# Kernel optimization log

Hardware: AMD Instinct MI355X
Metric: run time of the kernel (lower is better)

The kernel has to match this reference:

```python
import jax, jax.numpy as jnp
import numpy as np
from jax import lax

EPS = 1e-5
GROUPS = 8
TDVD_RANGE = 10
SCALE = 1.0
SCALE_FACTOR = 0.5


def setup_inputs() -> dict:
    key = jax.random.key(0)
    k1, k2 = jax.random.split(key)
    x = jax.random.normal(k1, (2, 16, 64, 128, 128), dtype=jnp.float32)
    gn_weight = jnp.ones((16,), dtype=jnp.float32)
    gn_bias = jnp.zeros((16,), dtype=jnp.float32)
    threshold = jnp.ones((1,), dtype=jnp.float32)  # torch fills with 1.0
    conv_weight = jax.random.normal(k2, (16, 16, 3, 3, 3), dtype=jnp.float32) * 0.05
    return {"x": x, "gn_weight": gn_weight, "gn_bias": gn_bias,
            "threshold": threshold, "conv_weight": conv_weight}


def _group_norm(x, w, b):
    B, C, D, H, W = x.shape
    xr = x.reshape(B, GROUPS, C // GROUPS, D, H, W)
    mean = xr.mean(axis=(2, 3, 4, 5), keepdims=True)
    var = xr.var(axis=(2, 3, 4, 5), keepdims=True)
    xn = ((xr - mean) * lax.rsqrt(var + EPS)).reshape(B, C, D, H, W)
    return xn * w.reshape(1, C, 1, 1, 1) + b.reshape(1, C, 1, 1, 1)


def _tdvd_histogram(x):
    # reverseint(x * scale * scale_factor) counted into 21 bins [-10..10], as %.
    y = x * (SCALE * SCALE_FACTOR)
    v = jnp.ceil(y * (y >= 0)) + jnp.floor(y * (y <= 0))
    idx = (v + TDVD_RANGE).astype(jnp.int32)
    valid = (idx >= 0) & (idx <= 2 * TDVD_RANGE)
    hist = jnp.zeros((2 * TDVD_RANGE + 1,), jnp.float32).at[
        jnp.clip(idx, 0, 2 * TDVD_RANGE)].add(jnp.where(valid, 1.0, 0.0))
    return hist / x.size * 100.0


def _threshold_func(x, threshold):
    thr = (threshold[0] + 0.0) / SCALE  # zero_point=0, scale=1.0
    t = jnp.transpose(x, (2, 0, 1, 3, 4))  # [D,B,C,H,W]
    front, back = t[:-1], t[1:]
    d = (back - front) / thr
    d = jnp.where(jnp.abs(d) > 1.0, d, 0.0)  # Hardshrink(1.0)
    d = d * lax.stop_gradient(thr)           # .item() detaches in torch
    out = jnp.concatenate([t[:1], front + d], axis=0)
    return jnp.transpose(out, (1, 2, 0, 3, 4))


def reference(x, gn_weight, gn_bias, threshold, conv_weight):
    x = jax.nn.relu(_group_norm(x, gn_weight, gn_bias))
    hist = _tdvd_histogram(x)
    x = _threshold_func(x, threshold)
    out = lax.conv_general_dilated(
        x, conv_weight, window_strides=(1, 1, 1),
        padding=((1, 1), (1, 1), (1, 1)),
        dimension_numbers=("NCDHW", "OIDHW", "NCDHW"))
    return out, hist
```

## Files before the change

### kernel.cpp

```cpp
#include <hip/hip_runtime.h>

typedef __attribute__((ext_vector_type(8))) short short8;
typedef __attribute__((ext_vector_type(4))) float f32x4;

#define GROUP_ELEMS 2097152
#define NBLK 64

__device__ inline short f2bf(float f) {
  unsigned u = __builtin_bit_cast(unsigned, f);
  unsigned r = (u + 0x7FFFu + ((u >> 16) & 1u)) >> 16;
  return (short)r;
}

__device__ inline void gload_lds16(const void* g, void* l) {
  __builtin_amdgcn_global_load_lds(
      (const __attribute__((address_space(1))) unsigned int*)g,
      (__attribute__((address_space(3))) unsigned int*)l, 16, 0, 0);
}

__global__ __launch_bounds__(256) void k1_partials(const float* __restrict__ x,
                                                   float2* __restrict__ partials,
                                                   const float* __restrict__ wgt,
                                                   unsigned short* __restrict__ fbw2,
                                                   int* __restrict__ hist,
                                                   unsigned int* __restrict__ dummy) {
  if (blockIdx.x == 1024) {
    int t0 = threadIdx.x;
    if (t0 < 21) hist[t0] = 0;
    #pragma unroll
    for (int it = 0; it < 4; ++it) {
      int t = t0 + it * 256;
      if (t < 960) {
        int f = t >> 6, lane = t & 63;
        int kd = f / 5, c = f - kd * 5;
        int m = lane & 15, g = lane >> 4;
        int icb = (g & 1) * 8, g2 = g >> 1;
        int tap = 2 * c + g2;
        short8 v;
        #pragma unroll
        for (int j = 0; j < 8; ++j)
          v[j] = (tap <= 8) ? f2bf(wgt[m * 432 + (icb + j) * 27 + kd * 9 + tap]) : (short)0;
        *(short8*)(fbw2 + t * 8) = v;
      }
      if (t >= 960 && t < 976) dummy[t - 960] = 0;
    }
    return;
  }
  int group = blockIdx.x >> 6;
  int blk = blockIdx.x & 63;
  const float4* p = (const float4*)(x + (size_t)group * GROUP_ELEMS + (size_t)blk * 32768);
  float sum = 0.f, sq = 0.f;
  for (int i = threadIdx.x; i < 8192; i += 256) {
    float4 v = p[i];
    sum += v.x + v.y + v.z + v.w;
    sq  += v.x*v.x + v.y*v.y + v.z*v.z + v.w*v.w;
  }
  for (int off = 32; off; off >>= 1) {
    sum += __shfl_down(sum, off, 64);
    sq  += __shfl_down(sq,  off, 64);
  }
  __shared__ float2 sw[4];
  int lane = threadIdx.x & 63, wid = threadIdx.x >> 6;
  if (lane == 0) sw[wid] = make_float2(sum, sq);
  __syncthreads();
  if (threadIdx.x == 0) {
    float s = 0.f, q = 0.f;
    for (int j = 0; j < 4; ++j) { s += sw[j].x; q += sw[j].y; }
    partials[blockIdx.x] = make_float2(s, q);
  }
}

__global__ __launch_bounds__(256) void k3_norm_thresh_hist(
    const float* __restrict__ x, const float* __restrict__ gw, const float* __restrict__ gb,
    const float* __restrict__ thrp, const float2* __restrict__ partials,
    unsigned short* __restrict__ z, int* __restrict__ hist) {
  __shared__ int sh[21];
  __shared__ float4 stf[8];
  __shared__ float red[64], redq[64];
  __shared__ unsigned sd[2][256];
  int t = threadIdx.x;
  if (t < 21) sh[t] = 0;
  int b = blockIdx.x >> 9;
  if (t < 64) {
    int gloc = t >> 3, j8 = t & 7;
    const float2* pp = partials + (b * 8 + gloc) * NBLK + j8 * 8;
    float s = 0.f, q = 0.f;
    #pragma unroll
    for (int k = 0; k < 8; ++k) { float2 pv = pp[k]; s += pv.x; q += pv.y; }
    red[t] = s; redq[t] = q;
  }
  __syncthreads();
  if (t < 8) {
    float s = 0.f, q = 0.f;
    #pragma unroll
    for (int k = 0; k < 8; ++k) { s += red[t * 8 + k]; q += redq[t * 8 + k]; }
    float mean = s / (float)GROUP_ELEMS;
    float var  = q / (float)GROUP_ELEMS - mean * mean;
    float rs = rsqrtf(var + 1e-5f);
    int c0 = t * 2;
    float A0 = gw[c0] * rs,     B0 = gb[c0] - mean * A0;
    float A1 = gw[c0 + 1] * rs, B1 = gb[c0 + 1] - mean * A1;
    stf[t] = make_float4(A0, B0, A1, B1);
  }
  __syncthreads();
  int hwl = t & 31, cp = t >> 5;
  int hw0 = (blockIdx.x & 511) * 32;
  int hw = hw0 + hwl;
  float4 st = stf[cp];
  float A0 = st.x, B0 = st.y, A1 = st.z, B1 = st.w;
  float thr = thrp[0];
  int c0 = cp * 2, c1 = c0 + 1;
  const float* px0 = x + (size_t)(b * 16 + c0) * 1048576 + hw;
  const float* px1 = x + (size_t)(b * 16 + c1) * 1048576 + hw;
  unsigned* zout = (unsigned*)z;
  const unsigned zbase = (unsigned)(b * 1048576 + hw0) * 8;
  const int wi = (cp << 5) | ((hwl + 4 * cp) & 31);
  const int ri = ((t & 7) << 5) | (((t >> 3) + 4 * (t & 7)) & 31);
  int c10 = 0, c11 = 0, c12 = 0;
  float xv0 = px0[0], xv1 = px1[0];
  float xm0 = px0[16384], xm1 = px1[16384];
  float yp0 = 0.f, yp1 = 0.f;
  for (int d = 0; d < 64; ++d) {
    float n0 = 0.f, n1 = 0.f;
    if (d < 62) { n0 = px0[(d + 2) * 16384]; n1 = px1[(d + 2) * 16384]; }
    float y0 = fmaxf(fmaf(xv0, A0, B0), 0.f);
    float y1 = fmaxf(fmaf(xv1, A1, B1), 0.f);
    float v0 = ceilf(0.5f * y0);
    if (v0 == 0.f) c10++; else if (v0 == 1.f) c11++; else if (v0 == 2.f) c12++;
    else if (v0 <= 10.f) atomicAdd(&sh[(int)v0 + 10], 1);
    float v1 = ceilf(0.5f * y1);
    if (v1 == 0.f) c10++; else if (v1 == 1.f) c11++; else if (v1 == 2.f) c12++;
    else if (v1 <= 10.f) atomicAdd(&sh[(int)v1 + 10], 1);
    float z0, z1;
    if (d == 0) { z0 = y0; z1 = y1; }
    else {
      z0 = (fabsf(y0 - yp0) > thr) ? y0 : yp0;
      z1 = (fabsf(y1 - yp1) > thr) ? y1 : yp1;
    }
    unsigned u = (unsigned)(unsigned short)f2bf(z0) | ((unsigned)(unsigned short)f2bf(z1) << 16);
    sd[d & 1][wi] = u;
    __syncthreads();
    zout[zbase + d * 131072 + t] = sd[d & 1][ri];
    yp0 = y0; yp1 = y1;
    xv0 = xm0; xv1 = xm1;
    xm0 = n0; xm1 = n1;
  }
  atomicAdd(&sh[10], c10);
  atomicAdd(&sh[11], c11);
  atomicAdd(&sh[12], c12);
  __syncthreads();
  if (t < 21) atomicAdd(&hist[t], sh[t]);
}

#define DT 8
#define PLANE 5440
__global__ __launch_bounds__(512, 4) void k4_conv(const unsigned short* __restrict__ z,
                                                  const unsigned short* __restrict__ fbw2,
                                                  const char* __restrict__ dummyc,
                                                  const int* __restrict__ hist,
                                                  float* __restrict__ out) {
  __shared__ unsigned short lz[2 * PLANE];
  const int t = threadIdx.x;
  if (blockIdx.x == 0 && blockIdx.y == 0 && blockIdx.z == 0 && t < 21)
    out[33554432u + t] = (float)hist[t] * (100.0f / 33554432.0f);
  const int lane = t & 63, wid = t >> 6;
  const int b = blockIdx.z;
  const int d0 = blockIdx.y * DT;
  const int h0 = (blockIdx.x >> 2) * 8, w0 = (blockIdx.x & 3) * 32;
  const int m = lane & 15, g = lane >> 4;
  const int icb = (g & 1) * 8, g2 = g >> 1;

  short8 fb2[15];
  #pragma unroll
  for (int f = 0; f < 15; ++f)
    fb2[f] = *(const short8*)(fbw2 + (f * 64 + lane) * 8);

  int tco[5];
  #pragma unroll
  for (int c = 0; c < 5; ++c) {
    int tap = 2 * c + g2; if (tap > 8) tap = 8;
    tco[c] = ((tap / 3) * 34 + (tap % 3)) * 16;
  }

  const char* zbc = (const char*)(z + (size_t)b * 16777216);

  const int cbA = wid * 64;
  const int cbB = (wid == 0) ? 512 : (wid == 1) ? 576 : 616;
  const bool hasB = (wid < 3);
  long long hobA, hobB; bool hvA, hvB;
  {
    int gi, r, rem, s, ig, hg, wg;
    gi = cbA + lane; r = gi / 68; rem = gi - r * 68; s = rem >> 1; ig = rem & 1;
    hg = h0 - 1 + r; wg = w0 - 1 + s;
    hvA = ((unsigned)hg < 128u) && ((unsigned)wg < 128u);
    hobA = ((long long)(hg * 128 + wg) * 16 + ig * 8) * 2;
    gi = cbB + lane; r = gi / 68; rem = gi - r * 68; s = rem >> 1; ig = rem & 1;
    hg = h0 - 1 + r; wg = w0 - 1 + s;
    hvB = ((unsigned)hg < 128u) && ((unsigned)wg < 128u);
    hobB = ((long long)(hg * 128 + wg) * 16 + ig * 8) * 2;
  }

  const f32x4 fzero = {0.f, 0.f, 0.f, 0.f};
  f32x4 A0[2], A1[2], A2[2];
  #pragma unroll
  for (int q = 0; q < 2; ++q) { A0[q] = fzero; A1[q] = fzero; A2[q] = fzero; }

  {
    const int dg = d0 - 1;
    const long long dgo = (long long)dg * 524288;
    const bool pd = (unsigned)dg < 64u;
    gload_lds16((pd && hvA) ? zbc + dgo + hobA : dummyc, &lz[cbA * 8]);
    if (hasB)
      gload_lds16((pd && hvB) ? zbc + dgo + hobB : dummyc, &lz[cbB * 8]);
  }
  __syncthreads();

#define BODY(PH, AS, AM, AN, DOJ2, DOJ1, DOJ0, DOLOAD, DOSTORE)                         \
  {                                                                                     \
    const int ph_ = (PH);                                                               \
    if (DOLOAD) {                                                                       \
      const int dg = d0 + ph_;                                                          \
      const long long dgo = (long long)dg * 524288;                                     \
      const bool pd = (unsigned)dg < 64u;                                               \
      const unsigned sl = ((unsigned)(ph_ + 1) & 1u) * PLANE;                           \
      gload_lds16((pd && hvA) ? zbc + dgo + hobA : dummyc, &lz[sl + cbA * 8]);          \
      if (hasB)                                                                         \
        gload_lds16((pd && hvB) ? zbc + dgo + hobB : dummyc, &lz[sl + cbB * 8]);        \
    }                                                                                   \
    const unsigned su = ((unsigned)ph_ & 1u) * PLANE;                                   \
    __builtin_amdgcn_s_setprio(1);                                                      \
    _Pragma("unroll")                                                                   \
    for (int q = 0; q < 2; ++q) {                                                       \
      const int hl = wid, wt = q;                                                       \
      const int qb = (hl * 34 + wt * 16 + m) * 16 + icb + (int)su;                      \
      _Pragma("unroll")                                                                 \
      for (int c = 0; c < 5; ++c) {                                                     \
        short8 a = *(const short8*)(&lz[qb + tco[c]]);                                  \
        if (DOJ2) AN[q] = __builtin_amdgcn_mfma_f32_16x16x32_bf16(a, fb2[c], AN[q], 0, 0, 0);      \
        if (DOJ1) AM[q] = __builtin_amdgcn_mfma_f32_16x16x32_bf16(a, fb2[5 + c], AM[q], 0, 0, 0);  \
        if (DOJ0) AS[q] = __builtin_amdgcn_mfma_f32_16x16x32_bf16(a, fb2[10 + c], AS[q], 0, 0, 0); \
      }                                                                                 \
    }                                                                                   \
    __builtin_amdgcn_s_setprio(0);                                                      \
    if (DOSTORE) {                                                                      \
      const int dd = d0 + ph_ - 2;                                                      \
      _Pragma("unroll")                                                                 \
      for (int q = 0; q < 2; ++q) {                                                     \
        const int hl = wid, wt = q;                                                     \
        float* op = out + (((size_t)(b * 16 + m) * 64 + dd) * 128 + (h0 + hl)) * 128    \
                    + w0 + wt * 16 + g * 4;                                             \
        *(float4*)op = make_float4(AS[q][0], AS[q][1], AS[q][2], AS[q][3]);             \
        AS[q] = fzero;                                                                  \
      }                                                                                 \
    }                                                                                   \
    __syncthreads();                                                                    \
  }

  BODY(0, A1, A2, A0, 1, 0, 0, 1, 0)
  BODY(1, A2, A0, A1, 1, 1, 0, 1, 0)
  BODY(2, A0, A1, A2, 1, 1, 1, 1, 1)
  #pragma unroll 1
  for (int pp = 3; pp <= 6; pp += 3) {
    BODY(pp,     A1, A2, A0, 1, 1, 1, 1, 1)
    BODY(pp + 1, A2, A0, A1, 1, 1, 1, 1, 1)
    BODY(pp + 2, A0, A1, A2, 1, 1, 1, 1, 1)
  }
  BODY(9, A1, A2, A0, 0, 0, 1, 0, 1)
#undef BODY
}

extern "C" void kernel_launch(void* const* d_in, const int* in_sizes, int n_in,
                              void* d_out, int out_size, void* d_ws, size_t ws_size,
                              hipStream_t stream) {
  (void)in_sizes; (void)n_in; (void)out_size; (void)ws_size;
  const float* x   = (const float*)d_in[0];
  const float* gw  = (const float*)d_in[1];
  const float* gb  = (const float*)d_in[2];
  const float* thr = (const float*)d_in[3];
  const float* cw  = (const float*)d_in[4];
  float* out = (float*)d_out;

  char* ws = (char*)d_ws;
  unsigned short* z = (unsigned short*)ws;
  float2* partials  = (float2*)(ws + (size_t)67108864);
  int*    hist      = (int*)  (ws + (size_t)67108864 + 8192 + 128);
  unsigned int* dummy = (unsigned int*)(ws + (size_t)67108864 + 8448);
  unsigned short* fbw2 = (unsigned short*)(ws + (size_t)67108864 + 16384);

  k1_partials<<<1025, 256, 0, stream>>>(x, partials, cw, fbw2, hist, dummy);
  k3_norm_thresh_hist<<<1024, 256, 0, stream>>>(x, gw, gb, thr, partials, z, hist);
  k4_conv<<<dim3(64, 8, 2), 512, 0, stream>>>(z, fbw2, (const char*)dummy, hist, out);
}
```

Baseline: 122.5 us.

## Quad-buffer conv input planes and process two depth planes per barrier

Grows the LDS staging buffer from two to four depth planes and restructures the conv pipeline to load two planes and compute two planes between each block barrier. This halves the number of __syncthreads and gives more prefetch distance to hide global-to-LDS load latency. The cost is twice the LDS per block (about 43KB), which may cut the number of resident blocks below the launch_bounds target of 4.

```diff
diff --git a/kernel.cpp b/kernel.cpp
--- a/kernel.cpp
+++ b/kernel.cpp
@@ -159,7 +159,7 @@
                                                   const char* __restrict__ dummyc,
                                                   const int* __restrict__ hist,
                                                   float* __restrict__ out) {
-  __shared__ unsigned short lz[2 * PLANE];
+  __shared__ unsigned short lz[4 * PLANE];
   const int t = threadIdx.x;
   if (blockIdx.x == 0 && blockIdx.y == 0 && blockIdx.z == 0 && t < 21)
     out[33554432u + t] = (float)hist[t] * (100.0f / 33554432.0f);
@@ -205,29 +205,20 @@
   #pragma unroll
   for (int q = 0; q < 2; ++q) { A0[q] = fzero; A1[q] = fzero; A2[q] = fzero; }
 
-  {
-    const int dg = d0 - 1;
-    const long long dgo = (long long)dg * 524288;
-    const bool pd = (unsigned)dg < 64u;
-    gload_lds16((pd && hvA) ? zbc + dgo + hobA : dummyc, &lz[cbA * 8]);
-    if (hasB)
-      gload_lds16((pd && hvB) ? zbc + dgo + hobB : dummyc, &lz[cbB * 8]);
-  }
-  __syncthreads();
-
-#define BODY(PH, AS, AM, AN, DOJ2, DOJ1, DOJ0, DOLOAD, DOSTORE)                         \
+#define STAGE(P)                                                                        \
   {                                                                                     \
-    const int ph_ = (PH);                                                               \
-    if (DOLOAD) {                                                                       \
-      const int dg = d0 + ph_;                                                          \
-      const long long dgo = (long long)dg * 524288;                                     \
-      const bool pd = (unsigned)dg < 64u;                                               \
-      const unsigned sl = ((unsigned)(ph_ + 1) & 1u) * PLANE;                           \
-      gload_lds16((pd && hvA) ? zbc + dgo + hobA : dummyc, &lz[sl + cbA * 8]);          \
-      if (hasB)                                                                         \
-        gload_lds16((pd && hvB) ? zbc + dgo + hobB : dummyc, &lz[sl + cbB * 8]);        \
-    }                                                                                   \
-    const unsigned su = ((unsigned)ph_ & 1u) * PLANE;                                   \
+    const int dg = d0 - 1 + (P);                                                        \
+    const long long dgo = (long long)dg * 524288;                                       \
+    const bool pd = (unsigned)dg < 64u;                                                 \
+    const unsigned sl = ((unsigned)(P) & 3u) * PLANE;                                   \
+    gload_lds16((pd && hvA) ? zbc + dgo + hobA : dummyc, &lz[sl + cbA * 8]);            \
+    if (hasB)                                                                           \
+      gload_lds16((pd && hvB) ? zbc + dgo + hobB : dummyc, &lz[sl + cbB * 8]);          \
+  }
+
+#define PC(P, AS, AM, AN, DOJ2, DOJ1, DOJ0, DOSTORE)                                    \
+  {                                                                                     \
+    const unsigned su = ((unsigned)(P) & 3u) * PLANE;                                   \
     __builtin_amdgcn_s_setprio(1);                                                      \
     _Pragma("unroll")                                                                   \
     for (int q = 0; q < 2; ++q) {                                                       \
@@ -243,7 +234,7 @@
     }                                                                                   \
     __builtin_amdgcn_s_setprio(0);                                                      \
     if (DOSTORE) {                                                                      \
-      const int dd = d0 + ph_ - 2;                                                      \
+      const int dd = d0 + (P) - 2;                                                      \
       _Pragma("unroll")                                                                 \
       for (int q = 0; q < 2; ++q) {                                                     \
         const int hl = wid, wt = q;                                                     \
@@ -253,20 +244,30 @@
         AS[q] = fzero;                                                                  \
       }                                                                                 \
     }                                                                                   \
-    __syncthreads();                                                                    \
-  }
-
-  BODY(0, A1, A2, A0, 1, 0, 0, 1, 0)
-  BODY(1, A2, A0, A1, 1, 1, 0, 1, 0)
-  BODY(2, A0, A1, A2, 1, 1, 1, 1, 1)
-  #pragma unroll 1
-  for (int pp = 3; pp <= 6; pp += 3) {
-    BODY(pp,     A1, A2, A0, 1, 1, 1, 1, 1)
-    BODY(pp + 1, A2, A0, A1, 1, 1, 1, 1, 1)
-    BODY(pp + 2, A0, A1, A2, 1, 1, 1, 1, 1)
-  }
-  BODY(9, A1, A2, A0, 0, 0, 1, 0, 1)
-#undef BODY
+  }
+
+  STAGE(0) STAGE(1)
+  __syncthreads();
+  STAGE(2) STAGE(3)
+  PC(0, A1, A2, A0, 1, 0, 0, 0)
+  PC(1, A2, A0, A1, 1, 1, 0, 0)
+  __syncthreads();
+  STAGE(4) STAGE(5)
+  PC(2, A0, A1, A2, 1, 1, 1, 1)
+  PC(3, A1, A2, A0, 1, 1, 1, 1)
+  __syncthreads();
+  STAGE(6) STAGE(7)
+  PC(4, A2, A0, A1, 1, 1, 1, 1)
+  PC(5, A0, A1, A2, 1, 1, 1, 1)
+  __syncthreads();
+  STAGE(8) STAGE(9)
+  PC(6, A1, A2, A0, 1, 1, 1, 1)
+  PC(7, A2, A0, A1, 1, 1, 1, 1)
+  __syncthreads();
+  PC(8, A0, A1, A2, 1, 1, 1, 1)
+  PC(9, A1, A2, A0, 0, 0, 1, 1)
+#undef STAGE
+#undef PC
 }
 
 extern "C" void kernel_launch(void* const* d_in, const int* in_sizes, int n_in,
```

Measured after the change: 120.5 us, median of 2. Within noise of the previous version (-1.6%).
